# Kernel optimization log

Measured on AMD Instinct MI355X. Metric: run time of the kernel, lower is better.

The kernel has to match this reference:

```python
import jax, jax.numpy as jnp
import numpy as np

B, S, D, H, HD = 2, 2048, 1024, 16, 64
K, L = 1024, 4  # num_codes, vq_levels


def setup_inputs() -> dict:
    key = jax.random.key(0)
    ks = jax.random.split(key, 12)
    w = lambda k, shape: jax.random.normal(k, shape, jnp.float32) * 0.02
    return {
        "x": jax.random.normal(ks[0], (B, S, D), jnp.float32),
        "ln1_g": jnp.ones((D,), jnp.float32), "ln1_b": jnp.zeros((D,), jnp.float32),
        "wq": w(ks[1], (D, D)), "wk": w(ks[2], (D, D)), "wv": w(ks[3], (D, D)),
        "wg": w(ks[4], (D, D)), "wo": w(ks[5], (D, D)),
        "ln2_g": jnp.ones((D,), jnp.float32), "ln2_b": jnp.zeros((D,), jnp.float32),
        "w1": w(ks[6], (D, 4 * D)), "b1": jnp.zeros((4 * D,), jnp.float32),
        "w2": w(ks[7], (4 * D, D)), "b2": jnp.zeros((D,), jnp.float32),
        "ln3_g": jnp.ones((D,), jnp.float32), "ln3_b": jnp.zeros((D,), jnp.float32),
        "codebooks": jax.random.uniform(ks[8], (L, K, D), jnp.float32, -1.0 / K, 1.0 / K),
    }


def _ln(x, g, b):
    m = jnp.mean(x, -1, keepdims=True)
    v = jnp.var(x, -1, keepdims=True)
    return (x - m) / jnp.sqrt(v + 1e-5) * g + b


def _rope(x):  # x: [B, S, H, HD]
    hd = x.shape[-1]
    inv = 1.0 / (10000.0 ** (jnp.arange(0, hd, 2, dtype=jnp.float32) / hd))
    t = jnp.arange(x.shape[1], dtype=jnp.float32)
    f = jnp.einsum('i,j->ij', t, inv)               # [S, HD/2]
    emb = jnp.concatenate([f, f], -1)               # [S, HD]
    cos = jnp.cos(emb)[None, :, None, :]
    sin = jnp.sin(emb)[None, :, None, :]
    x1, x2 = jnp.split(x, 2, -1)
    rot = jnp.concatenate([-x2, x1], -1)
    return x * cos + rot * sin


def reference(x, ln1_g, ln1_b, wq, wk, wv, wg, wo, ln2_g, ln2_b,
              w1, b1, w2, b2, ln3_g, ln3_b, codebooks):
    # --- retention sub-block (pre-LN) ---
    h = _ln(x, ln1_g, ln1_b)
    q = (h @ wq).reshape(B, S, H, HD)
    k = (h @ wk).reshape(B, S, H, HD)
    v = (h @ wv).reshape(B, S, H, HD)
    q, k = _rope(q), _rope(k)
    q, k, v = (a.transpose(0, 2, 1, 3) for a in (q, k, v))  # [B,H,S,HD]
    i = jnp.arange(S)
    dmask = jnp.tril(i[:, None] - i[None, :]).astype(jnp.float32)  # [S,S], >=0
    gamma = (1.0 - jnp.exp2(-5.0 - jnp.arange(H, dtype=jnp.float32)))[:, None, None]
    decay = (gamma ** dmask) * jnp.tril(jnp.ones((S, S), jnp.float32))  # [H,S,S]
    ret = jnp.einsum('bhqd,bhkd->bhqk', q, k) / np.sqrt(HD).astype(np.float32) * decay
    o = jnp.einsum('bhqk,bhkd->bhqd', ret, v).transpose(0, 2, 1, 3).reshape(B, S, D)
    g = jax.nn.silu(h @ wg)
    x = x + (o * g) @ wo
    # --- MLP sub-block (pre-LN) ---
    h2 = _ln(x, ln2_g, ln2_b)
    x = x + (jax.nn.gelu(h2 @ w1 + b1, approximate=False) @ w2 + b2)
    # --- residual vector quantizer ---
    xn = _ln(x, ln3_g, ln3_b)
    residual, total = xn, jnp.zeros_like(xn)
    ql, el = 0.0, 0.0
    for lvl in range(L):
        cb = codebooks[lvl]                         # [K, D]
        flat = residual.reshape(-1, D)              # [B*S, D]
        d2 = (jnp.sum(flat ** 2, 1, keepdims=True)
              + jnp.sum(cb ** 2, 1) - 2.0 * flat @ cb.T)
        idx = jnp.argmin(d2, 1)
        quant = cb[idx].reshape(xn.shape)
        ql = ql + jnp.mean((quant - jax.lax.stop_gradient(residual)) ** 2)
        el = el + jnp.mean((jax.lax.stop_gradient(quant) - residual) ** 2)
        total = total + quant
        residual = residual - jax.lax.stop_gradient(quant)
    final = xn + jax.lax.stop_gradient(total - xn)  # straight-through
    return (x + final, ql / L, el / L)
```

## Files before the change

### kernel.cpp

```cpp
#include <hip/hip_runtime.h>
#include <cstdint>
#include <cstddef>

#define DEV __device__ __forceinline__

typedef __attribute__((ext_vector_type(8))) short bf16x8;
typedef __attribute__((ext_vector_type(4))) float f32x4;

typedef const __attribute__((address_space(1))) void gl_void;
typedef __attribute__((address_space(3))) void lds_void;

DEV unsigned short f2bf(float f){
  union { float f; uint32_t u; } v; v.f = f;
  uint32_t r = v.u + 0x7FFFu + ((v.u >> 16) & 1u);
  return (unsigned short)(r >> 16);
}
DEV float bf2f(unsigned short u){
  union { uint32_t u; float f; } v; v.u = ((uint32_t)u) << 16; return v.f;
}
DEV uint32_t packbf2(float a, float b){
  return (uint32_t)f2bf(a) | ((uint32_t)f2bf(b) << 16);
}

__global__ void ln_kernel(const float* __restrict__ x, const float* __restrict__ gw,
                          const float* __restrict__ bw, unsigned short* __restrict__ obf,
                          float* __restrict__ of32)
{
  const int row = blockIdx.x, t = threadIdx.x;
  const float4 v = ((const float4*)(x + (size_t)row*1024))[t];
  float s  = v.x + v.y + v.z + v.w;
  float s2 = v.x*v.x + v.y*v.y + v.z*v.z + v.w*v.w;
  #pragma unroll
  for (int o = 32; o >= 1; o >>= 1){ s += __shfl_down(s, o); s2 += __shfl_down(s2, o); }
  __shared__ float red[8];
  const int w = t >> 6, ln = t & 63;
  if (ln == 0){ red[w] = s; red[4+w] = s2; }
  __syncthreads();
  const float fs  = red[0]+red[1]+red[2]+red[3];
  const float fs2 = red[4]+red[5]+red[6]+red[7];
  const float mean = fs * (1.0f/1024.0f);
  const float var  = fs2 * (1.0f/1024.0f) - mean*mean;
  const float rstd = rsqrtf(var + 1e-5f);
  const float4 gv = ((const float4*)gw)[t];
  const float4 bv = ((const float4*)bw)[t];
  float4 o4;
  o4.x = (v.x-mean)*rstd*gv.x + bv.x;
  o4.y = (v.y-mean)*rstd*gv.y + bv.y;
  o4.z = (v.z-mean)*rstd*gv.z + bv.z;
  o4.w = (v.w-mean)*rstd*gv.w + bv.w;
  if (of32) ((float4*)(of32 + (size_t)row*1024))[t] = o4;
  ushort4 ob; ob.x = f2bf(o4.x); ob.y = f2bf(o4.y); ob.z = f2bf(o4.z); ob.w = f2bf(o4.w);
  ((ushort4*)(obf + (size_t)row*1024))[t] = ob;
}

struct Ptr5 { const float* p[5]; };
__global__ void transpose_cvt5(Ptr5 in, unsigned short* __restrict__ out)
{
  __shared__ float tile[32][33];
  const float* src = in.p[blockIdx.z];
  unsigned short* dst = out + (size_t)blockIdx.z*1048576;
  const int c0 = blockIdx.x*32, r0 = blockIdx.y*32;
  const int tx = threadIdx.x & 31, ty = threadIdx.x >> 5;
  #pragma unroll
  for (int i = 0; i < 32; i += 8)
    tile[ty+i][tx] = src[(size_t)(r0+ty+i)*1024 + c0 + tx];
  __syncthreads();
  #pragma unroll
  for (int i = 0; i < 32; i += 8)
    dst[(size_t)(c0+ty+i)*1024 + r0 + tx] = f2bf(tile[tx][ty+i]);
}

__global__ void transpose_cvt(const float* __restrict__ in, unsigned short* __restrict__ out,
                              int R, int C)
{
  __shared__ float tile[32][33];
  const int c0 = blockIdx.x*32, r0 = blockIdx.y*32;
  const int tx = threadIdx.x & 31, ty = threadIdx.x >> 5;
  #pragma unroll
  for (int i = 0; i < 32; i += 8)
    tile[ty+i][tx] = in[(size_t)(r0+ty+i)*C + c0 + tx];
  __syncthreads();
  #pragma unroll
  for (int i = 0; i < 32; i += 8)
    out[(size_t)(c0+ty+i)*R + r0 + tx] = f2bf(tile[tx][ty+i]);
}

__global__ void cvtnorm_kernel(const float* __restrict__ cb, unsigned short* __restrict__ cbbf,
                               float* __restrict__ cbn2)
{
  const int code = blockIdx.x, t = threadIdx.x;
  const float4 v = ((const float4*)(cb + (size_t)code*1024))[t];
  ushort4 o; o.x = f2bf(v.x); o.y = f2bf(v.y); o.z = f2bf(v.z); o.w = f2bf(v.w);
  ((ushort4*)(cbbf + (size_t)code*1024))[t] = o;
  float s = v.x*v.x + v.y*v.y + v.z*v.z + v.w*v.w;
  #pragma unroll
  for (int off = 32; off >= 1; off >>= 1) s += __shfl_down(s, off);
  __shared__ float red[4];
  if ((t & 63) == 0) red[t >> 6] = s;
  __syncthreads();
  if (t == 0) cbn2[code] = red[0]+red[1]+red[2]+red[3];
}

__global__ void rope_tab(float2* __restrict__ rt)
{
  const int i = blockIdx.x*256 + threadIdx.x;
  const int s = i >> 5, j = i & 31;
  const float ang = (float)s * exp2f(-(float)j * 0.4152410118609203f);
  float sn, cs; sincosf(ang, &sn, &cs);
  rt[i] = make_float2(cs, sn);
}

template<int EPI>
__global__ __launch_bounds__(512, 2) void gemm256(
    const unsigned short* __restrict__ A, const unsigned short* __restrict__ BT,
    unsigned short* __restrict__ C, const float* __restrict__ bias,
    const float2* __restrict__ rt, int M, int N, int K)
{
  __shared__ __align__(16) unsigned short SH[49152];
  const int t = threadIdx.x;
  const int w = t >> 6, ln = t & 63, lg = ln >> 4, lc = ln & 15;
  const int wm = w >> 2, wn = w & 3;
  const int gx = gridDim.x, nwg = gridDim.x * gridDim.y;
  int lin = blockIdx.y * gx + blockIdx.x;
  lin = (lin >> 3) + (lin & 7) * (nwg >> 3);
  const int m0 = (lin / gx) * 256, n0 = (lin % gx) * 256;
  const int nkt = K >> 5;

  f32x4 acc[8][4] = {};

  auto stage = [&](int buf, int kt){
    #pragma unroll
    for (int isB = 0; isB < 2; ++isB){
      const unsigned short* src = isB ? BT : A;
      const int mb = isB ? n0 : m0;
      #pragma unroll
      for (int j = 0; j < 2; ++j){
        const int u = j*512 + t;
        const int ro = u >> 2;
        const int su = (u & 3) ^ ((ro >> 1) & 3);
        __builtin_amdgcn_global_load_lds(
          (gl_void*)(src + (size_t)(mb + ro)*K + (size_t)kt*32 + su*8),
          (lds_void*)&SH[buf*16384 + isB*8192 + (j*512 + (t & ~63))*8],
          16, 0, 0);
      }
    }
  };

  auto ldA = [&](int buf, int mf) -> bf16x8 {
    const int R = wm*128 + mf*16 + lc;
    const int cu = lg ^ ((R >> 1) & 3);
    return *(const bf16x8*)&SH[buf*16384 + (R*4 + cu)*8];
  };
  auto ldB = [&](int buf, int nf) -> bf16x8 {
    const int R = wn*64 + nf*16 + lc;
    const int cu = lg ^ ((R >> 1) & 3);
    return *(const bf16x8*)&SH[buf*16384 + 8192 + (R*4 + cu)*8];
  };

  stage(0, 0); stage(1, 1);
  asm volatile("s_waitcnt vmcnt(4)" ::: "memory");
  __builtin_amdgcn_s_barrier();

  for (int kt = 0; kt < nkt; ++kt){
    const int cur = kt % 3;
    const bool pf = (kt + 2 < nkt);
    bf16x8 aF[4], bF[4];

    if (pf) stage((kt + 2) % 3, kt + 2);
    #pragma unroll
    for (int f = 0; f < 4; ++f){ aF[f] = ldA(cur, f); bF[f] = ldB(cur, f); }
    __builtin_amdgcn_s_barrier();
    __builtin_amdgcn_s_setprio(1);
    #pragma unroll
    for (int mf = 0; mf < 4; ++mf)
      #pragma unroll
      for (int nf = 0; nf < 4; ++nf)
        acc[mf][nf] = __builtin_amdgcn_mfma_f32_16x16x32_bf16(aF[mf], bF[nf], acc[mf][nf], 0, 0, 0);
    __builtin_amdgcn_s_setprio(0);
    asm volatile("s_waitcnt lgkmcnt(0)" ::: "memory");
    __builtin_amdgcn_s_barrier();

    #pragma unroll
    for (int f = 0; f < 4; ++f) aF[f] = ldA(cur, 4 + f);
    __builtin_amdgcn_s_barrier();
    __builtin_amdgcn_s_setprio(1);
    #pragma unroll
    for (int mf = 0; mf < 4; ++mf)
      #pragma unroll
      for (int nf = 0; nf < 4; ++nf)
        acc[4+mf][nf] = __builtin_amdgcn_mfma_f32_16x16x32_bf16(aF[mf], bF[nf], acc[4+mf][nf], 0, 0, 0);
    __builtin_amdgcn_s_setprio(0);
    asm volatile("s_waitcnt lgkmcnt(0)" ::: "memory");
    if (pf) asm volatile("s_waitcnt vmcnt(4)" ::: "memory");
    else    asm volatile("s_waitcnt vmcnt(0)" ::: "memory");
    __builtin_amdgcn_s_barrier();
  }

  unsigned short* wls = &SH[w*1024];
  const int mrow = m0 + wm*128, ncol = n0 + wn*64;
  const int rr0 = ln >> 3, cc0 = (ln & 7)*8;
  if constexpr (EPI == 3){
    const int sect = ncol >> 10;
    unsigned short* outp = C + (size_t)sect*4194304;
    const int cbase = ncol & 1023;
    #pragma unroll
    for (int mf = 0; mf < 8; ++mf){
      #pragma unroll
      for (int r = 0; r < 4; ++r){
        const int row = mrow + mf*16 + lg*4 + r;
        const int s_ = row & 2047;
        #pragma unroll
        for (int nf = 0; nf < 4; ++nf){
          const int c1 = cbase + nf*16 + lc;
          float v = acc[mf][nf][r];
          if (sect <= 1){
            const float2 cs = rt[(s_ << 5) + (c1 & 31)];
            const float vp = acc[mf][nf ^ 2][r];
            v = (c1 & 32) ? (v*cs.x + vp*cs.y) : (v*cs.x - vp*cs.y);
          } else if (sect == 3){
            v = v * (1.0f / (1.0f + __expf(-v)));
          }
          wls[(lg*4+r)*64 + nf*16 + lc] = f2bf(v);
        }
      }
      #pragma unroll
      for (int i = 0; i < 2; ++i){
        const int rr = rr0 + 8*i;
        const bf16x8 vv = *(const bf16x8*)&wls[rr*64 + cc0];
        *(bf16x8*)(outp + (size_t)(mrow + mf*16 + rr)*1024 + cbase + cc0) = vv;
      }
    }
  } else {
    #pragma unroll
    for (int mf = 0; mf < 8; ++mf){
      #pragma unroll
      for (int r = 0; r < 4; ++r){
        #pragma unroll
        for (int nf = 0; nf < 4; ++nf){
          const int col = ncol + nf*16 + lc;
          float v = acc[mf][nf][r] + bias[col];
          v = 0.5f * v * (1.0f + erff(v * 0.70710678118654752f));
          wls[(lg*4+r)*64 + nf*16 + lc] = f2bf(v);
        }
      }
      #pragma unroll
      for (int i = 0; i < 2; ++i){
        const int rr = rr0 + 8*i;
        const bf16x8 vv = *(const bf16x8*)&wls[rr*64 + cc0];
        *(bf16x8*)(C + (size_t)(mrow + mf*16 + rr)*N + ncol + cc0) = vv;
      }
    }
  }
}

template<int EPI, bool BIAS, bool RES, bool OUTBF, int NSPLIT>
__global__ __launch_bounds__(256, 2) void gemm64_bt(
    const unsigned short* __restrict__ A, const unsigned short* __restrict__ BT,
    void* __restrict__ Cv, const float* __restrict__ bias, const float* __restrict__ resid,
    int M, int N, int K)
{
  __shared__ __align__(16) unsigned short As[3][64*64];
  __shared__ __align__(16) unsigned short Bs[3][128*64];
  const int t = threadIdx.x;
  const int w = t >> 6, ln = t & 63, lg = ln >> 4, lc = ln & 15;
  const int gx = gridDim.x, nwg = gridDim.x * gridDim.y;
  int lin = blockIdx.y * gx + blockIdx.x;
  lin = (lin >> 3) + (lin & 7) * (nwg >> 3);
  const int bx = lin % gx, by = lin / gx;
  const int m0 = by * 64, n0 = bx * 128;
  const int wr = (w >> 1) * 32, wc = (w & 1) * 64;
  f32x4 acc[2][4] = {};
  const int nkt = (K >> 6) / NSPLIT;
  const int ktb = (NSPLIT > 1) ? blockIdx.z * nkt : 0;

  auto stage = [&](int buf, int kt){
    #pragma unroll
    for (int c = 0; c < 2; ++c){
      const int chunk = c*256 + t;
      const int row = chunk >> 3;
      const int kb = (((chunk & 7) << 4) ^ ((row & 7) << 4)) >> 1;
      __builtin_amdgcn_global_load_lds(
          (gl_void*)(A + (size_t)(m0+row)*K + (size_t)(ktb+kt)*64 + kb),
          (lds_void*)&As[buf][(c*256 + w*64)*8], 16, 0, 0);
    }
    #pragma unroll
    for (int c = 0; c < 4; ++c){
      const int chunk = c*256 + t;
      const int row = chunk >> 3;
      const int kb = (((chunk & 7) << 4) ^ ((row & 7) << 4)) >> 1;
      __builtin_amdgcn_global_load_lds(
          (gl_void*)(BT + (size_t)(n0+row)*K + (size_t)(ktb+kt)*64 + kb),
          (lds_void*)&Bs[buf][(c*256 + w*64)*8], 16, 0, 0);
    }
  };

  stage(0, 0); stage(1, 1);
  asm volatile("s_waitcnt vmcnt(6)" ::: "memory");
  __builtin_amdgcn_s_barrier();

  for (int kt = 0; kt < nkt; ++kt){
    const int cur = kt % 3;
    const bool pf = (kt + 2 < nkt);
    if (pf) stage((kt + 2) % 3, kt + 2);
    __builtin_amdgcn_s_setprio(1);
    #pragma unroll
    for (int ks = 0; ks < 2; ++ks){
      bf16x8 af[2], bfr[4];
      #pragma unroll
      for (int i = 0; i < 2; ++i){
        const int rowA = wr + i*16 + lc;
        const int colA = (((ks<<6) + (lg<<4)) ^ ((rowA & 7) << 4)) >> 1;
        af[i] = *(const bf16x8*)&As[cur][rowA*64 + colA];
      }
      #pragma unroll
      for (int i = 0; i < 4; ++i){
        const int rowB = wc + i*16 + lc;
        const int colB = (((ks<<6) + (lg<<4)) ^ ((rowB & 7) << 4)) >> 1;
        bfr[i] = *(const bf16x8*)&Bs[cur][rowB*64 + colB];
      }
      #pragma unroll
      for (int m = 0; m < 2; ++m)
        #pragma unroll
        for (int n = 0; n < 4; ++n)
          acc[m][n] = __builtin_amdgcn_mfma_f32_16x16x32_bf16(af[m], bfr[n], acc[m][n], 0, 0, 0);
    }
    __builtin_amdgcn_s_setprio(0);
    asm volatile("s_waitcnt lgkmcnt(0)" ::: "memory");
    if (pf) asm volatile("s_waitcnt vmcnt(6)" ::: "memory");
    else    asm volatile("s_waitcnt vmcnt(0)" ::: "memory");
    __builtin_amdgcn_s_barrier();
  }

  if constexpr (EPI == 4){
    #pragma unroll
    for (int m = 0; m < 2; ++m){
      #pragma unroll
      for (int r = 0; r < 4; ++r){
        float best = 3.4e38f; int bi = 0;
        #pragma unroll
        for (int n = 0; n < 4; ++n){
          const int col = n0 + wc + n*16 + lc;
          const float d = bias[col] - 2.0f*acc[m][n][r];
          if (d < best){ best = d; bi = col; }
        }
        #pragma unroll
        for (int o = 1; o < 16; o <<= 1){
          const float ob = __shfl_xor(best, o);
          const int oi = __shfl_xor(bi, o);
          if (ob < best || (ob == best && oi < bi)){ best = ob; bi = oi; }
        }
        if (lc == 0){
          const int row = m0 + wr + m*16 + lg*4 + r;
          ((float2*)Cv)[row*16 + bx*2 + (w & 1)] = make_float2(best, (float)bi);
        }
      }
    }
    return;
  }

  float* Cp = (float*)Cv + (NSPLIT > 1 ? (size_t)blockIdx.z * (size_t)M * N : 0);
  #pragma unroll
  for (int m = 0; m < 2; ++m){
    #pragma unroll
    for (int n = 0; n < 4; ++n){
      #pragma unroll
      for (int r = 0; r < 4; ++r){
        const int row = m0 + wr + m*16 + lg*4 + r;
        const int col = n0 + wc + n*16 + lc;
        float v = acc[m][n][r];
        if constexpr (BIAS) v += bias[col];
        if constexpr (RES) v += resid[(size_t)row*N + col];
        if constexpr (OUTBF) ((unsigned short*)Cv)[(size_t)row*N + col] = f2bf(v);
        else                 Cp[(size_t)row*N + col] = v;
      }
    }
  }
}

__global__ void splitk_reduce(const float* __restrict__ p, const float* __restrict__ bias,
                              const float* __restrict__ resid, float* __restrict__ out)
{
  const int i = blockIdx.x*256 + threadIdx.x;
  const float4 a = ((const float4*)p)[i];
  const float4 b = ((const float4*)(p + 4194304))[i];
  const float4 rv = ((const float4*)resid)[i];
  const float4 bv = ((const float4*)bias)[i & 255];
  float4 o;
  o.x = a.x + b.x + rv.x + bv.x;
  o.y = a.y + b.y + rv.y + bv.y;
  o.z = a.z + b.z + rv.z + bv.z;
  o.w = a.w + b.w + rv.w + bv.w;
  ((float4*)out)[i] = o;
}

__global__ __launch_bounds__(256, 2) void chunk_sum(
    const unsigned short* __restrict__ kb, const unsigned short* __restrict__ vb,
    float* __restrict__ Tbuf)
{
  __shared__ unsigned short KT[64*72];
  __shared__ unsigned short VT[64*72];
  const int t = threadIdx.x, w = t >> 6, ln = t & 63, lg = ln >> 4, lc = ln & 15;
  const int blk = blockIdx.x;
  const int bh = blk >> 5, c = blk & 31;
  const int b = bh >> 4, hh = bh & 15;
  const float lg2g = log2f(1.0f - exp2f(-5.0f - (float)hh));
  #pragma unroll
  for (int ch = 0; ch < 2; ++ch){
    const int chunk = ch*256 + t;
    const int i = chunk >> 3, d0 = (chunk & 7)*8;
    const size_t gofs = ((size_t)(b*2048 + c*64 + i))*1024 + hh*64 + d0;
    const float wi = exp2f(lg2g * (float)(64 - i));
    union {uint4 u; unsigned short s[8];} kv, vv;
    kv.u = *(const uint4*)(kb + gofs);
    vv.u = *(const uint4*)(vb + gofs);
    #pragma unroll
    for (int j = 0; j < 8; ++j){
      KT[(d0+j)*72 + i] = f2bf(bf2f(kv.s[j]) * wi);
      VT[(d0+j)*72 + i] = vv.s[j];
    }
  }
  __syncthreads();
  f32x4 acc[4] = {};
  #pragma unroll
  for (int ks = 0; ks < 2; ++ks){
    const bf16x8 af = *(const bf16x8*)&KT[(w*16 + lc)*72 + ks*32 + lg*8];
    #pragma unroll
    for (int n = 0; n < 4; ++n){
      const bf16x8 bf = *(const bf16x8*)&VT[(n*16 + lc)*72 + ks*32 + lg*8];
      acc[n] = __builtin_amdgcn_mfma_f32_16x16x32_bf16(af, bf, acc[n], 0, 0, 0);
    }
  }
  float* out = Tbuf + (size_t)blk*4096;
  #pragma unroll
  for (int n = 0; n < 4; ++n)
    #pragma unroll
    for (int r = 0; r < 4; ++r)
      out[(w*16 + lg*4 + r)*64 + n*16 + lc] = acc[n][r];
}

__global__ void chunk_scan(const float* __restrict__ Tbuf, unsigned short* __restrict__ statesT)
{
  const int bh = blockIdx.x, q = blockIdx.y, t = threadIdx.x;
  const int hh = bh & 15;
  const float gamma = 1.0f - exp2f(-5.0f - (float)hh);
  const float g64 = exp2f(log2f(gamma) * 64.0f);
  float S[4] = {0.f, 0.f, 0.f, 0.f};
  const int dv = t >> 2;
  const int j0 = q*16 + (t & 3)*4;
  for (int c = 0; c < 32; ++c){
    const size_t base = ((size_t)(bh*32 + c))*4096;
    ushort4 p; p.x = f2bf(S[0]); p.y = f2bf(S[1]); p.z = f2bf(S[2]); p.w = f2bf(S[3]);
    *(ushort4*)(statesT + base + dv*64 + j0) = p;
    #pragma unroll
    for (int j = 0; j < 4; ++j)
      S[j] = g64*S[j] + Tbuf[base + (size_t)(j0 + j)*64 + dv];
  }
}

__global__ __launch_bounds__(256, 2) void retention_chunk(
    const unsigned short* __restrict__ qb, const unsigned short* __restrict__ kb,
    const unsigned short* __restrict__ vb, const unsigned short* __restrict__ gb,
    const unsigned short* __restrict__ statesT, unsigned short* __restrict__ og)
{
  __shared__ unsigned short VT[64*72];
  __shared__ unsigned short Pw[64*72];
  const int t = threadIdx.x, w = t >> 6, ln = t & 63, lg = ln >> 4, lc = ln & 15;
  const int blk = blockIdx.x;
  const int bh = blk >> 5, c = blk & 31;
  const int b = bh >> 4, hh = bh & 15;
  const float lg2g = log2f(1.0f - exp2f(-5.0f - (float)hh));
  float gpr[4];
  #pragma unroll
  for (int r = 0; r < 4; ++r) gpr[r] = exp2f(-lg2g * (float)r);
  const size_t rowbase = (size_t)(b*2048 + c*64);

  #pragma unroll
  for (int ch = 0; ch < 2; ++ch){
    const int chunk = ch*256 + t;
    const int i = chunk >> 3, d0 = (chunk & 7)*8;
    union {uint4 u; unsigned short s[8];} vv;
    vv.u = *(const uint4*)(vb + (rowbase + i)*1024 + hh*64 + d0);
    #pragma unroll
    for (int j = 0; j < 8; ++j) VT[(d0+j)*72 + i] = vv.s[j];
  }

  bf16x8 Qf[2], Kf[4][2];
  #pragma unroll
  for (int ks = 0; ks < 2; ++ks){
    union {uint4 u; bf16x8 f;} cv;
    cv.u = *(const uint4*)(qb + (rowbase + w*16 + lc)*1024 + hh*64 + ks*32 + lg*8);
    Qf[ks] = cv.f;
    #pragma unroll
    for (int mt = 0; mt < 4; ++mt){
      union {uint4 u; bf16x8 f;} kv;
      kv.u = *(const uint4*)(kb + (rowbase + mt*16 + lc)*1024 + hh*64 + ks*32 + lg*8);
      Kf[mt][ks] = kv.f;
    }
  }

  f32x4 st[4] = {};
  #pragma unroll
  for (int ks = 0; ks < 2; ++ks)
    #pragma unroll
    for (int mt = 0; mt < 4; ++mt)
      st[mt] = __builtin_amdgcn_mfma_f32_16x16x32_bf16(Kf[mt][ks], Qf[ks], st[mt], 0, 0, 0);

  __syncthreads();

  #pragma unroll
  for (int mt = 0; mt < 4; ++mt){
    const int kp = mt*16 + lg*4;
    const int qrow = w*16 + lc;
    const int delta0 = qrow - kp;
    const float dec0 = exp2f(lg2g * (float)delta0) * 0.125f;
    float vals[4];
    #pragma unroll
    for (int r = 0; r < 4; ++r)
      vals[r] = (delta0 >= r) ? st[mt][r] * dec0 * gpr[r] : 0.0f;
    uint2 pk; pk.x = packbf2(vals[0], vals[1]); pk.y = packbf2(vals[2], vals[3]);
    *(uint2*)&Pw[qrow*72 + kp] = pk;
  }

  f32x4 acc[4] = {};
  const unsigned short* Sbase = statesT + (size_t)blk*4096;
  #pragma unroll
  for (int ks = 0; ks < 2; ++ks)
    #pragma unroll
    for (int n = 0; n < 4; ++n){
      union {uint4 u; bf16x8 f;} sv;
      sv.u = *(const uint4*)(Sbase + (n*16 + lc)*64 + ks*32 + lg*8);
      acc[n] = __builtin_amdgcn_mfma_f32_16x16x32_bf16(Qf[ks], sv.f, acc[n], 0, 0, 0);
    }
  #pragma unroll
  for (int n = 0; n < 4; ++n)
    #pragma unroll
    for (int r = 0; r < 4; ++r)
      acc[n][r] *= exp2f(lg2g * (float)(w*16 + lg*4 + r)) * 0.125f;

  #pragma unroll
  for (int ks = 0; ks < 2; ++ks){
    const bf16x8 Pf = *(const bf16x8*)&Pw[(w*16 + lc)*72 + ks*32 + lg*8];
    #pragma unroll
    for (int n = 0; n < 4; ++n){
      const bf16x8 Vf = *(const bf16x8*)&VT[(n*16 + lc)*72 + ks*32 + lg*8];
      acc[n] = __builtin_amdgcn_mfma_f32_16x16x32_bf16(Pf, Vf, acc[n], 0, 0, 0);
    }
  }

  #pragma unroll
  for (int n = 0; n < 4; ++n){
    #pragma unroll
    for (int r = 0; r < 4; ++r){
      const size_t row = rowbase + w*16 + lg*4 + r;
      const int col = hh*64 + n*16 + lc;
      const float gv = bf2f(gb[row*1024 + col]);
      og[row*1024 + col] = f2bf(acc[n][r] * gv);
    }
  }
}

template<int FINAL>
__global__ void rvq_update3(const float* __restrict__ cb_l, const float2* __restrict__ partials,
                            const float* __restrict__ res_in, float* __restrict__ res_out,
                            unsigned short* __restrict__ resb, float* __restrict__ qlpart, int lvl,
                            const float* __restrict__ x2, const float* __restrict__ xn,
                            float* __restrict__ outf)
{
  const int m = blockIdx.x, t = threadIdx.x;
  __shared__ int sid;
  if (t == 0){
    float best = 3.4e38f; int bi = 0;
    #pragma unroll
    for (int p = 0; p < 16; ++p){
      const float2 pr = partials[m*16 + p];
      if (pr.x < best){ best = pr.x; bi = (int)pr.y; }
    }
    sid = bi;
  }
  __syncthreads();
  const int id = sid;
  const float4 qv = ((const float4*)(cb_l + (size_t)id*1024))[t];
  const float4 rv = ((const float4*)(res_in + (size_t)m*1024))[t];
  float4 nr; nr.x = rv.x - qv.x; nr.y = rv.y - qv.y; nr.z = rv.z - qv.z; nr.w = rv.w - qv.w;
  if constexpr (FINAL){
    const float4 a = ((const float4*)(x2 + (size_t)m*1024))[t];
    const float4 b = ((const float4*)(xn + (size_t)m*1024))[t];
    float4 o;
    o.x = a.x + b.x - nr.x;
    o.y = a.y + b.y - nr.y;
    o.z = a.z + b.z - nr.z;
    o.w = a.w + b.w - nr.w;
    ((float4*)(outf + (size_t)m*1024))[t] = o;
  } else {
    ((float4*)(res_out + (size_t)m*1024))[t] = nr;
    ushort4 nb; nb.x = f2bf(nr.x); nb.y = f2bf(nr.y); nb.z = f2bf(nr.z); nb.w = f2bf(nr.w);
    ((ushort4*)(resb + (size_t)m*1024))[t] = nb;
  }
  float s = nr.x*nr.x + nr.y*nr.y + nr.z*nr.z + nr.w*nr.w;
  #pragma unroll
  for (int o = 32; o >= 1; o >>= 1) s += __shfl_down(s, o);
  __shared__ float red[4];
  if ((t & 63) == 0) red[t >> 6] = s;
  __syncthreads();
  if (t == 0) qlpart[lvl*4096 + m] = red[0]+red[1]+red[2]+red[3];
}

__global__ void ql_final(const float* __restrict__ qlpart, float* __restrict__ outs)
{
  const int t = threadIdx.x;
  float s = 0.f;
  for (int i = t; i < 16384; i += 256) s += qlpart[i];
  #pragma unroll
  for (int o = 32; o >= 1; o >>= 1) s += __shfl_down(s, o);
  __shared__ float red[4];
  if ((t & 63) == 0) red[t >> 6] = s;
  __syncthreads();
  if (t == 0){
    const float q = (red[0]+red[1]+red[2]+red[3]) * (1.0f/4194304.0f) * 0.25f;
    outs[0] = q; outs[1] = q;
  }
}

extern "C" void kernel_launch(void* const* d_in, const int* in_sizes, int n_in,
                              void* d_out, int out_size, void* d_ws, size_t ws_size,
                              hipStream_t stream)
{
  const float* x     = (const float*)d_in[0];
  const float* ln1_g = (const float*)d_in[1];
  const float* ln1_b = (const float*)d_in[2];
  const float* wq    = (const float*)d_in[3];
  const float* wk    = (const float*)d_in[4];
  const float* wv    = (const float*)d_in[5];
  const float* wg    = (const float*)d_in[6];
  const float* wo    = (const float*)d_in[7];
  const float* ln2_g = (const float*)d_in[8];
  const float* ln2_b = (const float*)d_in[9];
  const float* w1    = (const float*)d_in[10];
  const float* b1    = (const float*)d_in[11];
  const float* w2    = (const float*)d_in[12];
  const float* b2    = (const float*)d_in[13];
  const float* ln3_g = (const float*)d_in[14];
  const float* ln3_b = (const float*)d_in[15];
  const float* cb    = (const float*)d_in[16];

  char* ws = (char*)d_ws;
  const size_t MB = 1024*1024;
  unsigned short* wqkvgT = (unsigned short*)(ws + 0*MB);
  unsigned short* w1T  = (unsigned short*)(ws + 10*MB);
  unsigned short* w2T  = (unsigned short*)(ws + 18*MB);
  unsigned short* cbbf = (unsigned short*)(ws + 26*MB);
  float* cbn2     = (float*)(ws + 34*MB);
  float* qlpart   = (float*)(ws + 34*MB + 16*1024);
  float2* partials= (float2*)(ws + 34*MB + 128*1024);
  unsigned short* hbf  = (unsigned short*)(ws + 35*MB);
  unsigned short* qbuf = (unsigned short*)(ws + 43*MB);
  unsigned short* kbuf = (unsigned short*)(ws + 51*MB);
  unsigned short* vbuf = (unsigned short*)(ws + 59*MB);
  unsigned short* gbuf = (unsigned short*)(ws + 67*MB);
  float* skbuf  = (float*)(ws + 43*MB);
  unsigned short* ogb  = (unsigned short*)(ws + 75*MB);
  float* x1     = (float*)(ws + 83*MB);
  unsigned short* h2   = (unsigned short*)(ws + 99*MB);
  unsigned short* a1   = (unsigned short*)(ws + 107*MB);
  float* x2     = (float*)(ws + 139*MB);
  float* Tbuf   = (float*)(ws + 139*MB);
  float* xnf    = (float*)(ws + 155*MB);
  unsigned short* statesT = (unsigned short*)(ws + 155*MB);
  unsigned short* resb = (unsigned short*)(ws + 171*MB);
  float2* rtab  = (float2*)(ws + 179*MB);
  float* resw   = (float*)(ws + 187*MB);

  float* outf = (float*)d_out;

  Ptr5 p5; p5.p[0]=wq; p5.p[1]=wk; p5.p[2]=wv; p5.p[3]=wg; p5.p[4]=wo;
  hipLaunchKernelGGL(transpose_cvt5, dim3(32,32,5), dim3(256), 0, stream, p5, wqkvgT);
  hipLaunchKernelGGL(transpose_cvt, dim3(128,32), dim3(256), 0, stream, w1, w1T, 1024, 4096);
  hipLaunchKernelGGL(transpose_cvt, dim3(32,128), dim3(256), 0, stream, w2, w2T, 4096, 1024);
  hipLaunchKernelGGL(cvtnorm_kernel, dim3(4096), dim3(256), 0, stream, cb, cbbf, cbn2);
  hipLaunchKernelGGL(rope_tab, dim3(256), dim3(256), 0, stream, rtab);

  hipLaunchKernelGGL(ln_kernel, dim3(4096), dim3(256), 0, stream, x, ln1_g, ln1_b, hbf, (float*)nullptr);
  hipLaunchKernelGGL((gemm256<3>), dim3(16,16), dim3(512), 0, stream,
                     hbf, wqkvgT, qbuf, (const float*)nullptr, (const float2*)rtab, 4096, 4096, 1024);
  hipLaunchKernelGGL(chunk_sum,  dim3(1024), dim3(256), 0, stream, kbuf, vbuf, Tbuf);
  hipLaunchKernelGGL(chunk_scan, dim3(32,4), dim3(256), 0, stream, Tbuf, statesT);
  hipLaunchKernelGGL(retention_chunk, dim3(1024), dim3(256), 0, stream,
                     qbuf, kbuf, vbuf, gbuf, statesT, ogb);
  hipLaunchKernelGGL((gemm64_bt<0,false,true,false,1>), dim3(8,64), dim3(256), 0, stream,
                     ogb, wqkvgT + 4194304, (void*)x1, (const float*)nullptr, x, 4096, 1024, 1024);

  hipLaunchKernelGGL(ln_kernel, dim3(4096), dim3(256), 0, stream, x1, ln2_g, ln2_b, h2, (float*)nullptr);
  hipLaunchKernelGGL((gemm256<2>), dim3(16,16), dim3(512), 0, stream,
                     h2, w1T, a1, b1, (const float2*)rtab, 4096, 4096, 1024);
  hipLaunchKernelGGL((gemm64_bt<0,false,false,false,2>), dim3(8,64,2), dim3(256), 0, stream,
                     a1, w2T, (void*)skbuf, (const float*)nullptr, (const float*)nullptr, 4096, 1024, 4096);
  hipLaunchKernelGGL(splitk_reduce, dim3(4096), dim3(256), 0, stream, skbuf, b2, x1, x2);

  hipLaunchKernelGGL(ln_kernel, dim3(4096), dim3(256), 0, stream, x2, ln3_g, ln3_b, resb, xnf);
  for (int lvl = 0; lvl < 4; ++lvl){
    hipLaunchKernelGGL((gemm64_bt<4,false,false,false,1>), dim3(8,64), dim3(256), 0, stream,
                       resb, cbbf + (size_t)lvl*1048576, (void*)partials,
                       cbn2 + lvl*1024, (const float*)nullptr, 4096, 1024, 1024);
    if (lvl < 3)
      hipLaunchKernelGGL((rvq_update3<0>), dim3(4096), dim3(256), 0, stream,
                         cb + (size_t)lvl*1048576, partials,
                         (lvl == 0) ? xnf : resw, resw, resb, qlpart, lvl,
                         (const float*)nullptr, (const float*)nullptr, (float*)nullptr);
    else
      hipLaunchKernelGGL((rvq_update3<1>), dim3(4096), dim3(256), 0, stream,
                         cb + (size_t)lvl*1048576, partials,
                         resw, (float*)nullptr, (unsigned short*)nullptr, qlpart, lvl,
                         x2, xnf, outf);
  }

  hipLaunchKernelGGL(ql_final, dim3(1), dim3(256), 0, stream, qlpart, outf + 4194304);
}
```

Before: 426.8 us.

## Restructure 256x256 GEMM into half-tile 8-wave ping-pong schedule with swizzled epilogue

The large GEMM now uses a BK=64 two-buffer scheme in which A and B tiles are split into 128-row halves. Each half is staged separately and interleaved with quarter-tile MFMA blocks, so global-to-LDS loads overlap compute at a finer grain. The epilogue is rewritten to stage bf16 results in a swizzled LDS slab and apply RoPE on packed 8-wide vectors. The small gemm64 kernel switches from a triple-buffered, setprio-scheduled pipeline to plain double buffering with __syncthreads and allows three workgroups per CU. This trades prefetch depth for occupancy and adds more barriers to the big kernel, and rounding to bf16 before the RoPE rotation may change numerics slightly.

```diff
diff --git a/kernel.cpp b/kernel.cpp
--- a/kernel.cpp
+++ b/kernel.cpp
@@ -116,7 +116,7 @@
     unsigned short* __restrict__ C, const float* __restrict__ bias,
     const float2* __restrict__ rt, int M, int N, int K)
 {
-  __shared__ __align__(16) unsigned short SH[49152];
+  __shared__ __align__(16) unsigned short SH[65536];
   const int t = threadIdx.x;
   const int w = t >> 6, ln = t & 63, lg = ln >> 4, lc = ln & 15;
   const int wm = w >> 2, wn = w & 3;
@@ -124,143 +124,175 @@
   int lin = blockIdx.y * gx + blockIdx.x;
   lin = (lin >> 3) + (lin & 7) * (nwg >> 3);
   const int m0 = (lin / gx) * 256, n0 = (lin % gx) * 256;
-  const int nkt = K >> 5;
-
-  f32x4 acc[8][4] = {};
-
-  auto stage = [&](int buf, int kt){
-    #pragma unroll
-    for (int isB = 0; isB < 2; ++isB){
-      const unsigned short* src = isB ? BT : A;
-      const int mb = isB ? n0 : m0;
+  const int NT = K >> 6;
+  const int nit = NT >> 1;
+
+  f32x4 acc[2][2][4][2] = {};
+  bf16x8 aF[4][2], bF[2][2];
+
+  auto stageHT = [&](int d, int isB, int h, int kt){
+    const unsigned short* src = isB ? BT : A;
+    const int mb = (isB ? n0 : m0) + h*128;
+    const int base16 = isB*4096 + d*2048 + h*1024;
+    #pragma unroll
+    for (int j = 0; j < 2; ++j){
+      const int o = j*512 + t;
+      const int wu = o & 63;
+      const int r16 = wu >> 2, cu = wu & 3;
+      const int s = o >> 6;
+      const int rg = s >> 1, cg = s & 1;
+      const int row = rg*16 + r16;
+      const int srcu = cg*4 + (cu ^ ((r16 & 8) >> 2));
+      __builtin_amdgcn_global_load_lds(
+        (gl_void*)(src + (size_t)(mb + row)*K + (size_t)kt*64 + srcu*8),
+        (lds_void*)&SH[(base16 + j*512 + (t & ~63))*8], 16, 0, 0);
+    }
+  };
+
+  auto ldA = [&](int d, int mh, int mf, int ks) -> bf16x8 {
+    const int u = d*2048 + mh*1024 + ((wm*4+mf)*2 + ks)*64 + lc*4 + (lg ^ ((lc & 8) >> 2));
+    return *(const bf16x8*)&SH[u*8];
+  };
+  auto ldB = [&](int d, int nh, int nf, int ks) -> bf16x8 {
+    const int u = 4096 + d*2048 + nh*1024 + ((wn*2+nf)*2 + ks)*64 + lc*4 + (lg ^ ((lc & 8) >> 2));
+    return *(const bf16x8*)&SH[u*8];
+  };
+
+#define RD_A(d, mh) { _Pragma("unroll") for (int mf = 0; mf < 4; ++mf){ \
+    aF[mf][0] = ldA(d, mh, mf, 0); aF[mf][1] = ldA(d, mh, mf, 1); } }
+#define RD_B(d, nh) { _Pragma("unroll") for (int nf = 0; nf < 2; ++nf){ \
+    bF[nf][0] = ldB(d, nh, nf, 0); bF[nf][1] = ldB(d, nh, nf, 1); } }
+#define MM(mh, nh) { \
+    __builtin_amdgcn_s_setprio(1); \
+    _Pragma("unroll") for (int mf = 0; mf < 4; ++mf) \
+      _Pragma("unroll") for (int nf = 0; nf < 2; ++nf){ \
+        acc[mh][nh][mf][nf] = __builtin_amdgcn_mfma_f32_16x16x32_bf16(aF[mf][0], bF[nf][0], acc[mh][nh][mf][nf], 0, 0, 0); \
+        acc[mh][nh][mf][nf] = __builtin_amdgcn_mfma_f32_16x16x32_bf16(aF[mf][1], bF[nf][1], acc[mh][nh][mf][nf], 0, 0, 0); } \
+    __builtin_amdgcn_s_setprio(0); }
+#define BAR()   __builtin_amdgcn_s_barrier()
+#define LGKM0() asm volatile("s_waitcnt lgkmcnt(0)" ::: "memory")
+
+  stageHT(0,0,0,0); stageHT(0,0,1,0); stageHT(0,1,0,0); stageHT(0,1,1,0);
+  stageHT(1,0,0,1); stageHT(1,1,1,1);
+  asm volatile("s_waitcnt vmcnt(4)" ::: "memory");
+  BAR();
+
+  for (int it = 0; it < nit; ++it){
+    const int v = 2*it + 1, up = 2*it + 2, vp = 2*it + 3;
+    const bool hu = (up < NT), hv = (vp < NT);
+
+    RD_A(0,0); RD_B(0,0);
+    stageHT(1,0,1,v);
+    BAR(); LGKM0(); MM(0,0); BAR();
+
+    RD_B(0,1);
+    stageHT(1,1,0,v);
+    BAR(); LGKM0(); MM(0,1); BAR();
+
+    RD_A(0,1);
+    if (hu) stageHT(0,0,0,up);
+    BAR(); LGKM0(); MM(1,1); BAR();
+
+    RD_B(0,0);
+    if (hu) stageHT(0,1,1,up);
+    BAR(); LGKM0(); MM(1,0);
+    if (hu) asm volatile("s_waitcnt vmcnt(4)" ::: "memory");
+    else    asm volatile("s_waitcnt vmcnt(0)" ::: "memory");
+    BAR();
+
+    RD_A(1,0); RD_B(1,0);
+    if (hu) stageHT(0,0,1,up);
+    BAR(); LGKM0(); MM(0,0); BAR();
+
+    RD_B(1,1);
+    if (hu) stageHT(0,1,0,up);
+    BAR(); LGKM0(); MM(0,1); BAR();
+
+    RD_A(1,1);
+    if (hv) stageHT(1,0,0,vp);
+    BAR(); LGKM0(); MM(1,1); BAR();
+
+    RD_B(1,0);
+    if (hv) stageHT(1,1,1,vp);
+    BAR(); LGKM0(); MM(1,0);
+    if (hv) asm volatile("s_waitcnt vmcnt(4)" ::: "memory");
+    else    asm volatile("s_waitcnt vmcnt(0)" ::: "memory");
+    BAR();
+  }
+#undef RD_A
+#undef RD_B
+#undef MM
+
+  const int sect = n0 >> 10;
+  unsigned short* outp3 = C + (size_t)sect*4194304;
+  const int cb1 = n0 & 1023;
+  unsigned short* slab = &SH[wm*4096];
+
+  #pragma unroll
+  for (int mh = 0; mh < 2; ++mh){
+    #pragma unroll
+    for (int mf = 0; mf < 4; ++mf){
+      BAR();
       #pragma unroll
-      for (int j = 0; j < 2; ++j){
-        const int u = j*512 + t;
-        const int ro = u >> 2;
-        const int su = (u & 3) ^ ((ro >> 1) & 3);
-        __builtin_amdgcn_global_load_lds(
-          (gl_void*)(src + (size_t)(mb + ro)*K + (size_t)kt*32 + su*8),
-          (lds_void*)&SH[buf*16384 + isB*8192 + (j*512 + (t & ~63))*8],
-          16, 0, 0);
-      }
-    }
-  };
-
-  auto ldA = [&](int buf, int mf) -> bf16x8 {
-    const int R = wm*128 + mf*16 + lc;
-    const int cu = lg ^ ((R >> 1) & 3);
-    return *(const bf16x8*)&SH[buf*16384 + (R*4 + cu)*8];
-  };
-  auto ldB = [&](int buf, int nf) -> bf16x8 {
-    const int R = wn*64 + nf*16 + lc;
-    const int cu = lg ^ ((R >> 1) & 3);
-    return *(const bf16x8*)&SH[buf*16384 + 8192 + (R*4 + cu)*8];
-  };
-
-  stage(0, 0); stage(1, 1);
-  asm volatile("s_waitcnt vmcnt(4)" ::: "memory");
-  __builtin_amdgcn_s_barrier();
-
-  for (int kt = 0; kt < nkt; ++kt){
-    const int cur = kt % 3;
-    const bool pf = (kt + 2 < nkt);
-    bf16x8 aF[4], bF[4];
-
-    if (pf) stage((kt + 2) % 3, kt + 2);
-    #pragma unroll
-    for (int f = 0; f < 4; ++f){ aF[f] = ldA(cur, f); bF[f] = ldB(cur, f); }
-    __builtin_amdgcn_s_barrier();
-    __builtin_amdgcn_s_setprio(1);
-    #pragma unroll
-    for (int mf = 0; mf < 4; ++mf)
+      for (int nh = 0; nh < 2; ++nh)
+        #pragma unroll
+        for (int nf = 0; nf < 2; ++nf)
+          #pragma unroll
+          for (int r = 0; r < 4; ++r){
+            const int rho = lg*4 + r;
+            const int c = nh*128 + wn*32 + nf*16 + lc;
+            float vv = acc[mh][nh][mf][nf][r];
+            if constexpr (EPI == 2){
+              vv += bias[n0 + c];
+              vv = 0.5f * vv * (1.0f + erff(vv * 0.70710678118654752f));
+            }
+            if constexpr (EPI == 3){ if (sect == 3) vv = vv * (1.0f / (1.0f + __expf(-vv))); }
+            slab[rho*256 + ((((c>>3) ^ (rho&3)))<<3) + (c&7)] = f2bf(vv);
+          }
+      LGKM0();
+      BAR();
+      const int rr = ln >> 2;
+      const int row = m0 + mh*128 + wm*64 + mf*16 + rr;
       #pragma unroll
-      for (int nf = 0; nf < 4; ++nf)
-        acc[mf][nf] = __builtin_amdgcn_mfma_f32_16x16x32_bf16(aF[mf], bF[nf], acc[mf][nf], 0, 0, 0);
-    __builtin_amdgcn_s_setprio(0);
-    asm volatile("s_waitcnt lgkmcnt(0)" ::: "memory");
-    __builtin_amdgcn_s_barrier();
-
-    #pragma unroll
-    for (int f = 0; f < 4; ++f) aF[f] = ldA(cur, 4 + f);
-    __builtin_amdgcn_s_barrier();
-    __builtin_amdgcn_s_setprio(1);
-    #pragma unroll
-    for (int mf = 0; mf < 4; ++mf)
-      #pragma unroll
-      for (int nf = 0; nf < 4; ++nf)
-        acc[4+mf][nf] = __builtin_amdgcn_mfma_f32_16x16x32_bf16(aF[mf], bF[nf], acc[4+mf][nf], 0, 0, 0);
-    __builtin_amdgcn_s_setprio(0);
-    asm volatile("s_waitcnt lgkmcnt(0)" ::: "memory");
-    if (pf) asm volatile("s_waitcnt vmcnt(4)" ::: "memory");
-    else    asm volatile("s_waitcnt vmcnt(0)" ::: "memory");
-    __builtin_amdgcn_s_barrier();
-  }
-
-  unsigned short* wls = &SH[w*1024];
-  const int mrow = m0 + wm*128, ncol = n0 + wn*64;
-  const int rr0 = ln >> 3, cc0 = (ln & 7)*8;
-  if constexpr (EPI == 3){
-    const int sect = ncol >> 10;
-    unsigned short* outp = C + (size_t)sect*4194304;
-    const int cbase = ncol & 1023;
-    #pragma unroll
-    for (int mf = 0; mf < 8; ++mf){
-      #pragma unroll
-      for (int r = 0; r < 4; ++r){
-        const int row = mrow + mf*16 + lg*4 + r;
-        const int s_ = row & 2047;
-        #pragma unroll
-        for (int nf = 0; nf < 4; ++nf){
-          const int c1 = cbase + nf*16 + lc;
-          float v = acc[mf][nf][r];
+      for (int kk = 0; kk < 2; ++kk){
+        const int cc = wn*64 + (ln & 3)*16 + kk*8;
+        const int u = cc >> 3;
+        const bf16x8 vown = *(const bf16x8*)&slab[rr*256 + ((u ^ (rr&3))<<3)];
+        if constexpr (EPI == 3){
           if (sect <= 1){
-            const float2 cs = rt[(s_ << 5) + (c1 & 31)];
-            const float vp = acc[mf][nf ^ 2][r];
-            v = (c1 & 32) ? (v*cs.x + vp*cs.y) : (v*cs.x - vp*cs.y);
-          } else if (sect == 3){
-            v = v * (1.0f / (1.0f + __expf(-v)));
+            const bf16x8 vpart = *(const bf16x8*)&slab[rr*256 + (((u^4) ^ (rr&3))<<3)];
+            const int s_ = row & 2047;
+            union { bf16x8 v; unsigned short s[8]; } ov, pv, res;
+            ov.v = vown; pv.v = vpart;
+            #pragma unroll
+            for (int j = 0; j < 8; ++j){
+              const int col = cc + j;
+              const float2 cs = rt[(s_ << 5) + (col & 31)];
+              const float a = bf2f(ov.s[j]), b = bf2f(pv.s[j]);
+              res.s[j] = f2bf((col & 32) ? (a*cs.x + b*cs.y) : (a*cs.x - b*cs.y));
+            }
+            *(bf16x8*)(outp3 + (size_t)row*1024 + cb1 + cc) = res.v;
+          } else {
+            *(bf16x8*)(outp3 + (size_t)row*1024 + cb1 + cc) = vown;
           }
-          wls[(lg*4+r)*64 + nf*16 + lc] = f2bf(v);
+        } else {
+          *(bf16x8*)(C + (size_t)row*N + n0 + cc) = vown;
         }
       }
-      #pragma unroll
-      for (int i = 0; i < 2; ++i){
-        const int rr = rr0 + 8*i;
-        const bf16x8 vv = *(const bf16x8*)&wls[rr*64 + cc0];
-        *(bf16x8*)(outp + (size_t)(mrow + mf*16 + rr)*1024 + cbase + cc0) = vv;
-      }
-    }
-  } else {
-    #pragma unroll
-    for (int mf = 0; mf < 8; ++mf){
-      #pragma unroll
-      for (int r = 0; r < 4; ++r){
-        #pragma unroll
-        for (int nf = 0; nf < 4; ++nf){
-          const int col = ncol + nf*16 + lc;
-          float v = acc[mf][nf][r] + bias[col];
-          v = 0.5f * v * (1.0f + erff(v * 0.70710678118654752f));
-          wls[(lg*4+r)*64 + nf*16 + lc] = f2bf(v);
-        }
-      }
-      #pragma unroll
-      for (int i = 0; i < 2; ++i){
-        const int rr = rr0 + 8*i;
-        const bf16x8 vv = *(const bf16x8*)&wls[rr*64 + cc0];
-        *(bf16x8*)(C + (size_t)(mrow + mf*16 + rr)*N + ncol + cc0) = vv;
-      }
-    }
-  }
+    }
+  }
+#undef BAR
+#undef LGKM0
 }
 
 template<int EPI, bool BIAS, bool RES, bool OUTBF, int NSPLIT>
-__global__ __launch_bounds__(256, 2) void gemm64_bt(
+__global__ __launch_bounds__(256, 3) void gemm64_bt(
     const unsigned short* __restrict__ A, const unsigned short* __restrict__ BT,
     void* __restrict__ Cv, const float* __restrict__ bias, const float* __restrict__ resid,
     int M, int N, int K)
 {
-  __shared__ __align__(16) unsigned short As[3][64*64];
-  __shared__ __align__(16) unsigned short Bs[3][128*64];
+  __shared__ __align__(16) unsigned short As[2][64*64];
+  __shared__ __align__(16) unsigned short Bs[2][128*64];
   const int t = threadIdx.x;
   const int w = t >> 6, ln = t & 63, lg = ln >> 4, lc = ln & 15;
   const int gx = gridDim.x, nwg = gridDim.x * gridDim.y;
@@ -294,15 +326,11 @@
     }
   };
 
-  stage(0, 0); stage(1, 1);
-  asm volatile("s_waitcnt vmcnt(6)" ::: "memory");
-  __builtin_amdgcn_s_barrier();
-
+  stage(0, 0);
+  __syncthreads();
   for (int kt = 0; kt < nkt; ++kt){
-    const int cur = kt % 3;
-    const bool pf = (kt + 2 < nkt);
-    if (pf) stage((kt + 2) % 3, kt + 2);
-    __builtin_amdgcn_s_setprio(1);
+    const int cur = kt & 1;
+    if (kt + 1 < nkt) stage(cur ^ 1, kt + 1);
     #pragma unroll
     for (int ks = 0; ks < 2; ++ks){
       bf16x8 af[2], bfr[4];
@@ -324,11 +352,7 @@
         for (int n = 0; n < 4; ++n)
           acc[m][n] = __builtin_amdgcn_mfma_f32_16x16x32_bf16(af[m], bfr[n], acc[m][n], 0, 0, 0);
     }
-    __builtin_amdgcn_s_setprio(0);
-    asm volatile("s_waitcnt lgkmcnt(0)" ::: "memory");
-    if (pf) asm volatile("s_waitcnt vmcnt(6)" ::: "memory");
-    else    asm volatile("s_waitcnt vmcnt(0)" ::: "memory");
-    __builtin_amdgcn_s_barrier();
+    __syncthreads();
   }
 
   if constexpr (EPI == 4){
```

Result: faster. 404.7 us (-5.2%).
